# Optimization experiments

Hardware: AMD Instinct MI355X
Metric: run time of the kernel (lower is better)

The kernel has to match this reference:

```python
import jax, jax.numpy as jnp
import numpy as np

B, S, H = 2, 2048, 2048
NH, NKV, HD = 8, 2, 256
WIN = 512
EPS = 1e-6
WAV = 10000.0


def _rms_norm(x, scale=None, eps=EPS):
    # Gemma3n RMSNorm: normalize in float32 over last dim, optional learned scale.
    x32 = x.astype(jnp.float32)
    n = x32 * jax.lax.rsqrt(jnp.mean(x32 * x32, axis=-1, keepdims=True) + eps)
    if scale is not None:
        n = n * scale
    return n.astype(x.dtype)


def _rope(x):
    # keras-hub RotaryEmbedding (half-split rotation). x: [B, S, nheads, hd]
    s, hd = x.shape[1], x.shape[-1]
    inv_freq = 1.0 / (WAV ** (jnp.arange(0, hd, 2, dtype=jnp.float32) / hd))  # [hd/2]
    freqs = jnp.arange(s, dtype=jnp.float32)[:, None] * inv_freq[None, :]      # [S, hd/2]
    cos = jnp.cos(freqs)[None, :, None, :]
    sin = jnp.sin(freqs)[None, :, None, :]
    x1, x2 = jnp.split(x, 2, axis=-1)
    return jnp.concatenate([x1 * cos - x2 * sin, x2 * cos + x1 * sin], axis=-1)


def setup_inputs() -> dict:
    key = jax.random.key(0)
    ks = jax.random.split(key, 8)
    hidden_states = jax.random.normal(ks[0], (B, S, H), dtype=jnp.float32)
    # causal mask [B, S, S]
    causal = jnp.tril(jnp.ones((S, S), dtype=bool))
    attention_mask = jnp.broadcast_to(causal[None], (B, S, S))
    sd = 1.0 / np.sqrt(H)
    Wq = jax.random.normal(ks[1], (H, NH * HD), dtype=jnp.float32) * sd
    Wk = jax.random.normal(ks[2], (H, NKV * HD), dtype=jnp.float32) * sd
    Wv = jax.random.normal(ks[3], (H, NKV * HD), dtype=jnp.float32) * sd
    Wo = jax.random.normal(ks[4], (NH * HD, H), dtype=jnp.float32) * (1.0 / np.sqrt(NH * HD))
    q_scale = jnp.ones((HD,), jnp.float32) + 0.02 * jax.random.normal(ks[5], (HD,), dtype=jnp.float32)
    k_scale = jnp.ones((HD,), jnp.float32) + 0.02 * jax.random.normal(ks[6], (HD,), dtype=jnp.float32)
    return {"hidden_states": hidden_states, "attention_mask": attention_mask,
            "Wq": Wq, "Wk": Wk, "Wv": Wv, "Wo": Wo,
            "q_scale": q_scale, "k_scale": k_scale}


def reference(hidden_states, attention_mask, Wq, Wk, Wv, Wo, q_scale, k_scale):
    b, s, _ = hidden_states.shape
    # Q: proj -> per-head RMSNorm -> RoPE -> [B, NH, S, HD]
    q = (hidden_states @ Wq).reshape(b, s, NH, HD)
    q = jnp.transpose(_rope(_rms_norm(q, q_scale)), (0, 2, 1, 3))
    # K: proj -> RMSNorm -> RoPE; V: proj -> RMSNorm (no scale, no RoPE)
    k = (hidden_states @ Wk).reshape(b, s, NKV, HD)
    k = jnp.transpose(_rope(_rms_norm(k, k_scale)), (0, 2, 1, 3))
    v = jnp.transpose(_rms_norm((hidden_states @ Wv).reshape(b, s, NKV, HD)), (0, 2, 1, 3))
    # GQA repeat_kv (groups = NH // NKV)
    g = NH // NKV
    k = jnp.repeat(k, g, axis=1)
    v = jnp.repeat(v, g, axis=1)
    # scores with scaling = 1.0 (as in source)
    scores = jnp.einsum('bhqd,bhkd->bhqk', q, k)
    # sliding-window band AND user causal mask
    idx = jnp.arange(s)
    band = jnp.abs(idx[:, None] - idx[None, :]) <= (WIN - 1)  # [S, S]
    mask = attention_mask.astype(bool) & band[None]           # [B, S, S]
    scores = jnp.where(mask[:, None], scores, -1e9)
    attn = jax.nn.softmax(scores, axis=-1)
    out = jnp.einsum('bhqk,bhkd->bhqd', attn, v)
    out = jnp.transpose(out, (0, 2, 1, 3)).reshape(b, s, NH * HD)
    return out @ Wo
```

## Files before the change

kernel.cpp:

```cpp
#include <hip/hip_runtime.h>
#include <cstdint>
#include <cstddef>

typedef unsigned short u16;
typedef float floatx4 __attribute__((ext_vector_type(4)));
typedef __bf16 bf16x8 __attribute__((ext_vector_type(8)));

__device__ __forceinline__ u16 f2bf(float f) {
  union { float f; unsigned u; } v;
  v.f = f;
  unsigned u = v.u;
  u += 0x7FFFu + ((u >> 16) & 1u);
  return (u16)(u >> 16);
}
__device__ __forceinline__ float bf2f(u16 h) {
  union { unsigned u; float f; } v;
  v.u = ((unsigned)h) << 16;
  return v.f;
}

#define GLL16(g, l)                                                       \
  __builtin_amdgcn_global_load_lds(                                       \
      (const __attribute__((address_space(1))) void*)(g),                 \
      (__attribute__((address_space(3))) void*)(l), 16, 0, 0)


__global__ __launch_bounds__(256) void splitbf(const float* __restrict__ in,
                                               u16* __restrict__ oh,
                                               u16* __restrict__ ol, int n8) {
  int idx = blockIdx.x * 256 + threadIdx.x;
  if (idx >= n8) return;
  float x[8];
  *(float4*)&x[0] = *(const float4*)(in + (size_t)idx * 8);
  *(float4*)&x[4] = *(const float4*)(in + (size_t)idx * 8 + 4);
  u16 h[8], l[8];
#pragma unroll
  for (int j = 0; j < 8; ++j) {
    h[j] = f2bf(x[j]);
    l[j] = f2bf(x[j] - bf2f(h[j]));
  }
  *(uint4*)(oh + (size_t)idx * 8) = *(const uint4*)h;
  *(uint4*)(ol + (size_t)idx * 8) = *(const uint4*)l;
}

__global__ __launch_bounds__(256) void wtrans(const float* __restrict__ in,
                                              u16* __restrict__ out, int R,
                                              int C) {
  __shared__ u16 T[64][80];
  const int t = threadIdx.x;
  const int r0 = blockIdx.y * 64;
  const int c0 = blockIdx.x * 64;
#pragma unroll
  for (int p = 0; p < 4; ++p) {
    const int rl = (t >> 4) + p * 16;
    const int c4 = (t & 15) * 4;
    float4 v = *(const float4*)(in + (size_t)(r0 + rl) * C + c0 + c4);
    T[c4 + 0][rl] = f2bf(v.x);
    T[c4 + 1][rl] = f2bf(v.y);
    T[c4 + 2][rl] = f2bf(v.z);
    T[c4 + 3][rl] = f2bf(v.w);
  }
  __syncthreads();
#pragma unroll
  for (int p = 0; p < 2; ++p) {
    const int cl = (t >> 3) + p * 32;
    const int r8 = (t & 7) * 8;
    *(uint4*)(out + (size_t)(c0 + cl) * R + r0 + r8) =
        *(const uint4*)&T[cl][r8];
  }
}

__global__ __launch_bounds__(256) void gemm_bf16s2(
    const u16* __restrict__ Ah, const u16* __restrict__ Al,
    const u16* __restrict__ Bt, float* __restrict__ C, int M, int N, int K) {
  __shared__ u16 Ash[2][4096], Asl[2][4096], Bs[2][4096];
  const int tid = threadIdx.x;
  const int lane = tid & 63;
  const int wid = tid >> 6;
  const int g = lane >> 4, lc = lane & 15;
  const int gsw = g ^ ((lc >> 1) & 3);
  const int lbs = lc * 32 + gsw * 8;
  const int nwg = gridDim.x * gridDim.y;
  const int lin = blockIdx.y * gridDim.x + blockIdx.x;
  const int swz = (lin & 7) * (nwg >> 3) + (lin >> 3);
  const int bm = (swz / gridDim.x) * 128, bn = (swz % gridDim.x) * 128;
  const int wr = (wid >> 1) * 64, wc = (wid & 1) * 64;
  const int xk8 = (((tid & 3) ^ ((tid >> 3) & 3)) * 8);
  const size_t aoff = (size_t)(bm + (tid >> 2)) * K + xk8;
  const size_t boff = (size_t)(bn + (tid >> 2)) * K + xk8;

  floatx4 acc[4][4];
#pragma unroll
  for (int i = 0; i < 4; ++i)
#pragma unroll
    for (int j = 0; j < 4; ++j) acc[i][j] = floatx4{0.f, 0.f, 0.f, 0.f};

  GLL16(Ah + aoff, Ash[0] + tid * 8);
  GLL16(Ah + aoff + (size_t)64 * K, Ash[0] + 2048 + tid * 8);
  GLL16(Al + aoff, Asl[0] + tid * 8);
  GLL16(Al + aoff + (size_t)64 * K, Asl[0] + 2048 + tid * 8);
  GLL16(Bt + boff, Bs[0] + tid * 8);
  GLL16(Bt + boff + (size_t)64 * K, Bs[0] + 2048 + tid * 8);
  int cur = 0;

  for (int k0 = 0; k0 < K; k0 += 32) {
    __syncthreads();
    if (k0 + 32 < K) {
      const int kn = k0 + 32;
      GLL16(Ah + aoff + kn, Ash[cur ^ 1] + tid * 8);
      GLL16(Ah + aoff + (size_t)64 * K + kn, Ash[cur ^ 1] + 2048 + tid * 8);
      GLL16(Al + aoff + kn, Asl[cur ^ 1] + tid * 8);
      GLL16(Al + aoff + (size_t)64 * K + kn, Asl[cur ^ 1] + 2048 + tid * 8);
      GLL16(Bt + boff + kn, Bs[cur ^ 1] + tid * 8);
      GLL16(Bt + boff + (size_t)64 * K + kn, Bs[cur ^ 1] + 2048 + tid * 8);
    }
    bf16x8 afh[4], afl[4], bfr[4];
#pragma unroll
    for (int m = 0; m < 4; ++m) {
      afh[m] = *(const bf16x8*)(Ash[cur] + (wr + m * 16) * 32 + lbs);
      afl[m] = *(const bf16x8*)(Asl[cur] + (wr + m * 16) * 32 + lbs);
    }
#pragma unroll
    for (int n = 0; n < 4; ++n)
      bfr[n] = *(const bf16x8*)(Bs[cur] + (wc + n * 16) * 32 + lbs);
#pragma unroll
    for (int m = 0; m < 4; ++m)
#pragma unroll
      for (int n = 0; n < 4; ++n) {
        acc[m][n] = __builtin_amdgcn_mfma_f32_16x16x32_bf16(afh[m], bfr[n],
                                                            acc[m][n], 0, 0, 0);
        acc[m][n] = __builtin_amdgcn_mfma_f32_16x16x32_bf16(afl[m], bfr[n],
                                                            acc[m][n], 0, 0, 0);
      }
    cur ^= 1;
  }
#pragma unroll
  for (int m = 0; m < 4; ++m)
#pragma unroll
    for (int n = 0; n < 4; ++n) {
      float* Cp = C + (size_t)(bm + wr + m * 16 + g * 4) * N + bn + wc +
                  n * 16 + lc;
#pragma unroll
      for (int r = 0; r < 4; ++r) Cp[(size_t)r * N] = acc[m][n][r];
    }
}

__global__ __launch_bounds__(256) void gemm_bf16(const u16* __restrict__ A,
                                                 const u16* __restrict__ Bt,
                                                 float* __restrict__ C, int M,
                                                 int N, int K) {
  __shared__ u16 As[2][4096];
  __shared__ u16 Bs[2][4096];
  const int tid = threadIdx.x;
  const int lane = tid & 63;
  const int wid = tid >> 6;
  const int g = lane >> 4, lc = lane & 15;
  const int gsw = g ^ ((lc >> 1) & 3);
  const int lbs = lc * 32 + gsw * 8;
  const int nwg = gridDim.x * gridDim.y;
  const int lin = blockIdx.y * gridDim.x + blockIdx.x;
  const int swz = (lin & 7) * (nwg >> 3) + (lin >> 3);
  const int bm = (swz / gridDim.x) * 128, bn = (swz % gridDim.x) * 128;
  const int wr = (wid >> 1) * 64, wc = (wid & 1) * 64;
  const int xk8 = (((tid & 3) ^ ((tid >> 3) & 3)) * 8);
  const u16* Ag = A + (size_t)(bm + (tid >> 2)) * K + xk8;
  const u16* Bg = Bt + (size_t)(bn + (tid >> 2)) * K + xk8;

  floatx4 acc[4][4];
#pragma unroll
  for (int i = 0; i < 4; ++i)
#pragma unroll
    for (int j = 0; j < 4; ++j) acc[i][j] = floatx4{0.f, 0.f, 0.f, 0.f};

  GLL16(Ag, As[0] + tid * 8);
  GLL16(Ag + (size_t)64 * K, As[0] + 2048 + tid * 8);
  GLL16(Bg, Bs[0] + tid * 8);
  GLL16(Bg + (size_t)64 * K, Bs[0] + 2048 + tid * 8);
  int cur = 0;

  for (int k0 = 0; k0 < K; k0 += 32) {
    __syncthreads();
    if (k0 + 32 < K) {
      const int kn = k0 + 32;
      GLL16(Ag + kn, As[cur ^ 1] + tid * 8);
      GLL16(Ag + (size_t)64 * K + kn, As[cur ^ 1] + 2048 + tid * 8);
      GLL16(Bg + kn, Bs[cur ^ 1] + tid * 8);
      GLL16(Bg + (size_t)64 * K + kn, Bs[cur ^ 1] + 2048 + tid * 8);
    }
    bf16x8 af[4], bfr[4];
#pragma unroll
    for (int m = 0; m < 4; ++m)
      af[m] = *(const bf16x8*)(As[cur] + (wr + m * 16) * 32 + lbs);
#pragma unroll
    for (int n = 0; n < 4; ++n)
      bfr[n] = *(const bf16x8*)(Bs[cur] + (wc + n * 16) * 32 + lbs);
#pragma unroll
    for (int m = 0; m < 4; ++m)
#pragma unroll
      for (int n = 0; n < 4; ++n)
        acc[m][n] = __builtin_amdgcn_mfma_f32_16x16x32_bf16(af[m], bfr[n],
                                                            acc[m][n], 0, 0, 0);
    cur ^= 1;
  }
#pragma unroll
  for (int m = 0; m < 4; ++m)
#pragma unroll
    for (int n = 0; n < 4; ++n) {
      float* Cp = C + (size_t)(bm + wr + m * 16 + g * 4) * N + bn + wc +
                  n * 16 + lc;
#pragma unroll
      for (int r = 0; r < 4; ++r) Cp[(size_t)r * N] = acc[m][n][r];
    }
}

__global__ __launch_bounds__(128) void trigtab(float* __restrict__ ct,
                                               float* __restrict__ st) {
  const int s = blockIdx.x, fi = threadIdx.x;
  const float invf = expf((float)fi * (-9.210340371976184f / 128.f));
  float sv, cv;
  sincosf((float)s * invf, &sv, &cv);
  ct[s * 128 + fi] = cv;
  st[s * 128 + fi] = sv;
}

__global__ __launch_bounds__(256) void rmsrope2(
    const float* __restrict__ qproj, const float* __restrict__ kvproj,
    u16* __restrict__ qph, u16* __restrict__ qpl, u16* __restrict__ kph,
    u16* __restrict__ kpl, u16* __restrict__ vpk,
    const float* __restrict__ q_scale, const float* __restrict__ k_scale,
    const float* __restrict__ ct, const float* __restrict__ st) {
  __shared__ u16 nh[32][264], nl[32][264];
  const int t = threadIdx.x, lane = t & 63, w = t >> 6;
  const int blk = blockIdx.x;
  const int slot = blk % 12;
  const int rt = blk / 12;
  const int bs0 = rt * 32;
  const int b = bs0 >> 11;
  const int s0 = bs0 & 2047;
  const float* srcb;
  const float* scale = nullptr;
  int srccol, srcstride;
  bool rope;
  if (slot < 8) {
    srcb = qproj;
    srccol = slot * 256;
    srcstride = 2048;
    scale = q_scale;
    rope = true;
  } else if (slot < 10) {
    srcb = kvproj;
    srccol = (slot - 8) * 256;
    srcstride = 1024;
    scale = k_scale;
    rope = true;
  } else {
    srcb = kvproj;
    srccol = 512 + (slot - 10) * 256;
    srcstride = 1024;
    rope = false;
  }
  const int d0 = lane * 4;
  float4 sc4 = make_float4(1.f, 1.f, 1.f, 1.f);
  if (scale) sc4 = *(const float4*)(scale + d0);
  const int fi4 = (lane & 31) * 4;

#pragma unroll
  for (int rr = 0; rr < 8; ++rr) {
    const int r = w * 8 + rr;
    const int s = s0 + r;
    float4 x = *(const float4*)(srcb + (size_t)(bs0 + r) * srcstride + srccol +
                                d0);
    float ss = x.x * x.x + x.y * x.y + x.z * x.z + x.w * x.w;
#pragma unroll
    for (int off = 32; off; off >>= 1) ss += __shfl_xor(ss, off);
    const float inv = rsqrtf(ss * (1.f / 256.f) + 1e-6f);
    float4 n;
    n.x = x.x * inv * sc4.x;
    n.y = x.y * inv * sc4.y;
    n.z = x.z * inv * sc4.z;
    n.w = x.w * inv * sc4.w;
    if (rope) {
      float4 p;
      p.x = __shfl_xor(n.x, 32);
      p.y = __shfl_xor(n.y, 32);
      p.z = __shfl_xor(n.z, 32);
      p.w = __shfl_xor(n.w, 32);
      const float4 cv = *(const float4*)(ct + s * 128 + fi4);
      const float4 sv = *(const float4*)(st + s * 128 + fi4);
      if (lane < 32) {
        n.x = n.x * cv.x - p.x * sv.x;
        n.y = n.y * cv.y - p.y * sv.y;
        n.z = n.z * cv.z - p.z * sv.z;
        n.w = n.w * cv.w - p.w * sv.w;
      } else {
        n.x = n.x * cv.x + p.x * sv.x;
        n.y = n.y * cv.y + p.y * sv.y;
        n.z = n.z * cv.z + p.z * sv.z;
        n.w = n.w * cv.w + p.w * sv.w;
      }
    }
    const float nv[4] = {n.x, n.y, n.z, n.w};
#pragma unroll
    for (int j = 0; j < 4; ++j) {
      const u16 hh = f2bf(nv[j]);
      nh[r][d0 + j] = hh;
      nl[r][d0 + j] = f2bf(nv[j] - bf2f(hh));
    }
  }
  __syncthreads();

  if (slot < 8) {
    u16* dh = qph + (((size_t)(b * 8 + slot) * 128 + (s0 >> 4)) * 4096);
    u16* dl = qpl + (((size_t)(b * 8 + slot) * 128 + (s0 >> 4)) * 4096);
#pragma unroll
    for (int p = 0; p < 4; ++p) {
      const int gi = p * 256 + t;
      const int tile = gi >> 9, kc = (gi >> 6) & 7, lc2 = (gi >> 2) & 15,
                gg = gi & 3;
      const int row = tile * 16 + lc2, col = kc * 32 + gg * 8;
      *(uint4*)(dh + (size_t)gi * 8) = *(const uint4*)&nh[row][col];
      *(uint4*)(dl + (size_t)gi * 8) = *(const uint4*)&nl[row][col];
    }
  } else if (slot < 10) {
    const int kvh = slot - 8;
    u16* dh = kph + (((size_t)(b * 2 + kvh) * 64 + (s0 >> 5)) * 8192);
    u16* dl = kpl + (((size_t)(b * 2 + kvh) * 64 + (s0 >> 5)) * 8192);
#pragma unroll
    for (int p = 0; p < 4; ++p) {
      const int gi = p * 256 + t;
      const int kc = gi >> 7, hi = (gi >> 6) & 1, lc2 = (gi >> 2) & 15,
                gg = gi & 3;
      const int ggs = gg ^ ((lc2 >> 1) & 3);
      const int row = hi * 16 + lc2, col = kc * 32 + gg * 8;
      const size_t off = kc * 1024 + hi * 512 + lc2 * 32 + ggs * 8;
      *(uint4*)(dh + off) = *(const uint4*)&nh[row][col];
      *(uint4*)(dl + off) = *(const uint4*)&nl[row][col];
    }
  } else {
    const int kvh = slot - 10;
    u16* dv = vpk + (((size_t)(b * 2 + kvh) * 64 + (s0 >> 5)) * 8192);
#pragma unroll
    for (int p = 0; p < 4; ++p) {
      const int gi = p * 256 + t;
      const int di = gi >> 6, lc2 = (gi >> 2) & 15, gg = gi & 3;
      const int ggs = gg ^ ((lc2 >> 1) & 3);
      u16 tmp[8];
#pragma unroll
      for (int e = 0; e < 8; ++e) tmp[e] = nh[gg * 8 + e][di * 16 + lc2];
      *(uint4*)(dv + (size_t)(di * 512 + lc2 * 32 + ggs * 8)) =
          *(const uint4*)tmp;
    }
  }
}

__global__ __launch_bounds__(512) void attn_mfma4(
    const u16* __restrict__ qph, const u16* __restrict__ qpl,
    const u16* __restrict__ kph, const u16* __restrict__ kpl,
    const u16* __restrict__ vpk, u16* __restrict__ attnb) {
  __shared__ u16 KhB[2][8192], KlB[2][8192], VB[2][8192];
  __shared__ u16 Pl[8][640];
  const int tid = threadIdx.x, lane = tid & 63, wid = tid >> 6;
  const int g = lane >> 4, lc = lane & 15;
  const int lbu = lc * 32 + g * 8;
  const int lbs = lc * 32 + (g ^ ((lc >> 1) & 3)) * 8;
  const int lin = blockIdx.x;
  const int swz = (lin & 7) * 32 + (lin >> 3);
  const int qt = swz & 15;
  const int h = (swz >> 4) & 7;
  const int b = swz >> 7;
  const int kvh = h >> 2;
  const int i0b = qt * 128;
  const int i0 = i0b + wid * 16;

  bf16x8 qfh[8], qfl[8];
  {
    const size_t qtb = ((size_t)(b * 8 + h) * 128 + (i0 >> 4)) * 4096 + lbu;
#pragma unroll
    for (int kc = 0; kc < 8; ++kc) {
      qfh[kc] = *(const bf16x8*)(qph + qtb + kc * 512);
      qfl[kc] = *(const bf16x8*)(qpl + qtb + kc * 512);
    }
  }
  floatx4 o[16];
#pragma unroll
  for (int d = 0; d < 16; ++d) o[d] = floatx4{0.f, 0.f, 0.f, 0.f};
  float m_[4] = {-1e20f, -1e20f, -1e20f, -1e20f};
  float l_[4] = {0.f, 0.f, 0.f, 0.f};
  u16* pw = Pl[wid];

  const int jlo = (i0b >= 512) ? i0b - 512 : 0;
  const int nt = (i0b + 128 - jlo) >> 5;
  const size_t kvbase = (size_t)(b * 2 + kvh) * 64;
  const int t0 = jlo >> 5;

  {
    const size_t tb = (kvbase + t0) * 8192;
    GLL16(kph + tb + tid * 8, KhB[0] + tid * 8);
    GLL16(kph + tb + 4096 + tid * 8, KhB[0] + 4096 + tid * 8);
    GLL16(kpl + tb + tid * 8, KlB[0] + tid * 8);
    GLL16(kpl + tb + 4096 + tid * 8, KlB[0] + 4096 + tid * 8);
    GLL16(vpk + tb + tid * 8, VB[0] + tid * 8);
    GLL16(vpk + tb + 4096 + tid * 8, VB[0] + 4096 + tid * 8);
  }
  int cur = 0;

  for (int t = 0; t < nt; ++t) {
    __syncthreads();
    if (t + 1 < nt) {
      const size_t tb = (kvbase + t0 + t + 1) * 8192;
      GLL16(kph + tb + tid * 8, KhB[cur ^ 1] + tid * 8);
      GLL16(kph + tb + 4096 + tid * 8, KhB[cur ^ 1] + 4096 + tid * 8);
      GLL16(kpl + tb + tid * 8, KlB[cur ^ 1] + tid * 8);
      GLL16(kpl + tb + 4096 + tid * 8, KlB[cur ^ 1] + 4096 + tid * 8);
      GLL16(vpk + tb + tid * 8, VB[cur ^ 1] + tid * 8);
      GLL16(vpk + tb + 4096 + tid * 8, VB[cur ^ 1] + 4096 + tid * 8);
    }
    const int j0 = jlo + t * 32;
    if (!(j0 > i0 + 15 || j0 + 31 < i0 - 511)) {
      const u16* Kh = KhB[cur];
      const u16* Kl = KlB[cur];
      floatx4 s0 = floatx4{0.f, 0.f, 0.f, 0.f};
      floatx4 s1 = floatx4{0.f, 0.f, 0.f, 0.f};
      __builtin_amdgcn_s_setprio(1);
#pragma unroll
      for (int kc = 0; kc < 8; ++kc) {
        const bf16x8 kh0 = *(const bf16x8*)(Kh + kc * 1024 + lbs);
        const bf16x8 kh1 = *(const bf16x8*)(Kh + kc * 1024 + 512 + lbs);
        const bf16x8 kl0 = *(const bf16x8*)(Kl + kc * 1024 + lbs);
        const bf16x8 kl1 = *(const bf16x8*)(Kl + kc * 1024 + 512 + lbs);
        s0 = __builtin_amdgcn_mfma_f32_16x16x32_bf16(qfh[kc], kh0, s0, 0, 0, 0);
        s0 = __builtin_amdgcn_mfma_f32_16x16x32_bf16(qfh[kc], kl0, s0, 0, 0, 0);
        s0 = __builtin_amdgcn_mfma_f32_16x16x32_bf16(qfl[kc], kh0, s0, 0, 0, 0);
        s1 = __builtin_amdgcn_mfma_f32_16x16x32_bf16(qfh[kc], kh1, s1, 0, 0, 0);
        s1 = __builtin_amdgcn_mfma_f32_16x16x32_bf16(qfh[kc], kl1, s1, 0, 0, 0);
        s1 = __builtin_amdgcn_mfma_f32_16x16x32_bf16(qfl[kc], kh1, s1, 0, 0, 0);
      }
      __builtin_amdgcn_s_setprio(0);
      if (!(j0 + 31 <= i0 && (i0 + 15) - j0 <= 511)) {
        const int ja = j0 + lc, jb_ = j0 + 16 + lc;
#pragma unroll
        for (int r = 0; r < 4; ++r) {
          const int i = i0 + g * 4 + r;
          if (ja > i || i - ja > 511) s0[r] = -1e30f;
          if (jb_ > i || i - jb_ > 511) s1[r] = -1e30f;
        }
      }
      float rmax[4], p0[4], p1[4], sc[4], rs[4];
#pragma unroll
      for (int r = 0; r < 4; ++r) rmax[r] = fmaxf(s0[r], s1[r]);
#pragma unroll
      for (int off = 1; off < 16; off <<= 1)
#pragma unroll
        for (int r = 0; r < 4; ++r)
          rmax[r] = fmaxf(rmax[r], __shfl_xor(rmax[r], off));
#pragma unroll
      for (int r = 0; r < 4; ++r) {
        const float mn = fmaxf(m_[r], rmax[r]);
        sc[r] = __expf(m_[r] - mn);
        m_[r] = mn;
        p0[r] = __expf(s0[r] - mn);
        p1[r] = __expf(s1[r] - mn);
        rs[r] = p0[r] + p1[r];
      }
#pragma unroll
      for (int off = 1; off < 16; off <<= 1)
#pragma unroll
        for (int r = 0; r < 4; ++r) rs[r] += __shfl_xor(rs[r], off);
#pragma unroll
      for (int r = 0; r < 4; ++r) l_[r] = l_[r] * sc[r] + rs[r];
#pragma unroll
      for (int r = 0; r < 4; ++r) {
        pw[(g * 4 + r) * 40 + lc] = f2bf(p0[r]);
        pw[(g * 4 + r) * 40 + 16 + lc] = f2bf(p1[r]);
      }
#pragma unroll
      for (int d = 0; d < 16; ++d)
#pragma unroll
        for (int r = 0; r < 4; ++r) o[d][r] *= sc[r];
      const bf16x8 pf = *(const bf16x8*)(pw + lc * 40 + g * 8);
      const u16* Vt = VB[cur];
      __builtin_amdgcn_s_setprio(1);
#pragma unroll
      for (int d = 0; d < 16; ++d)
        o[d] = __builtin_amdgcn_mfma_f32_16x16x32_bf16(
            pf, *(const bf16x8*)(Vt + d * 512 + lbs), o[d], 0, 0, 0);
      __builtin_amdgcn_s_setprio(0);
    }
    cur ^= 1;
  }
  float rinv[4];
#pragma unroll
  for (int r = 0; r < 4; ++r) rinv[r] = 1.f / l_[r];
  u16* ob = attnb + (size_t)(b * 2048 + i0 + g * 4) * 2048 + h * 256 + lc;
#pragma unroll
  for (int d = 0; d < 16; ++d)
#pragma unroll
    for (int r = 0; r < 4; ++r)
      ob[(size_t)r * 2048 + d * 16] = f2bf(o[d][r] * rinv[r]);
}

extern "C" void kernel_launch(void* const* d_in, const int* in_sizes, int n_in,
                              void* d_out, int out_size, void* d_ws,
                              size_t ws_size, hipStream_t stream) {
  (void)in_sizes;
  (void)n_in;
  (void)out_size;
  (void)ws_size;
  const float* X = (const float*)d_in[0];
  const float* Wq = (const float*)d_in[2];
  const float* Wk = (const float*)d_in[3];
  const float* Wv = (const float*)d_in[4];
  const float* Wo = (const float*)d_in[5];
  const float* qs = (const float*)d_in[6];
  const float* ks = (const float*)d_in[7];
  float* out = (float*)d_out;
  char* ws = (char*)d_ws;

  float* kvproj = (float*)(ws);
  u16* attnb = (u16*)(ws);
  u16* Xh = (u16*)(ws + 16777216);
  u16* qph = Xh;
  u16* Xl = (u16*)(ws + 33554432);
  u16* qpl = Xl;
  u16* Wth = (u16*)(ws + 50331648);
  u16* kph = (u16*)(ws + 50331648);
  u16* kpl = (u16*)(ws + 54525952);
  u16* vpk = (u16*)(ws + 58720256);
  float* ct = (float*)(ws + 62914560);
  float* st = (float*)(ws + 63963136);
  u16* Wot = (u16*)(ws + 75497472);
  float* qproj = out;

  splitbf<<<4096, 256, 0, stream>>>(X, Xh, Xl, 1048576);
  wtrans<<<dim3(32, 32), 256, 0, stream>>>(Wq, Wth, 2048, 2048);
  wtrans<<<dim3(8, 32), 256, 0, stream>>>(Wk, Wth + (size_t)2048 * 2048, 2048,
                                          512);
  wtrans<<<dim3(8, 32), 256, 0, stream>>>(Wv, Wth + (size_t)2560 * 2048, 2048,
                                          512);
  wtrans<<<dim3(32, 32), 256, 0, stream>>>(Wo, Wot, 2048, 2048);
  gemm_bf16s2<<<dim3(16, 32), 256, 0, stream>>>(Xh, Xl, Wth, qproj, 4096, 2048,
                                                2048);
  gemm_bf16s2<<<dim3(8, 32), 256, 0, stream>>>(
      Xh, Xl, Wth + (size_t)2048 * 2048, kvproj, 4096, 1024, 2048);
  trigtab<<<2048, 128, 0, stream>>>(ct, st);
  rmsrope2<<<12 * 128, 256, 0, stream>>>(qproj, kvproj, qph, qpl, kph, kpl,
                                         vpk, qs, ks, ct, st);
  attn_mfma4<<<256, 512, 0, stream>>>(qph, qpl, kph, kpl, vpk, attnb);
  gemm_bf16<<<dim3(16, 32), 256, 0, stream>>>(attnb, Wot, out, 4096, 2048,
                                              2048);
}
```

Before: 299.1 us.

## Merge prep kernels, fuse QKV GEMMs, split score accumulators, stage attention output

```diff
diff --git a/kernel.cpp b/kernel.cpp
--- a/kernel.cpp
+++ b/kernel.cpp
@@ -24,32 +24,54 @@
       (const __attribute__((address_space(1))) void*)(g),                 \
       (__attribute__((address_space(3))) void*)(l), 16, 0, 0)
 
-
-__global__ __launch_bounds__(256) void splitbf(const float* __restrict__ in,
-                                               u16* __restrict__ oh,
-                                               u16* __restrict__ ol, int n8) {
-  int idx = blockIdx.x * 256 + threadIdx.x;
-  if (idx >= n8) return;
-  float x[8];
-  *(float4*)&x[0] = *(const float4*)(in + (size_t)idx * 8);
-  *(float4*)&x[4] = *(const float4*)(in + (size_t)idx * 8 + 4);
-  u16 h[8], l[8];
-#pragma unroll
-  for (int j = 0; j < 8; ++j) {
-    h[j] = f2bf(x[j]);
-    l[j] = f2bf(x[j] - bf2f(h[j]));
-  }
-  *(uint4*)(oh + (size_t)idx * 8) = *(const uint4*)h;
-  *(uint4*)(ol + (size_t)idx * 8) = *(const uint4*)l;
-}
-
-__global__ __launch_bounds__(256) void wtrans(const float* __restrict__ in,
-                                              u16* __restrict__ out, int R,
-                                              int C) {
+__global__ __launch_bounds__(256) void prep_all(
+    const float* __restrict__ X, u16* __restrict__ Xh, u16* __restrict__ Xl,
+    const float* __restrict__ Wq, const float* __restrict__ Wk,
+    const float* __restrict__ Wv, const float* __restrict__ Wo,
+    u16* __restrict__ Wth, u16* __restrict__ Wot, float* __restrict__ ct,
+    float* __restrict__ st) {
   __shared__ u16 T[64][80];
-  const int t = threadIdx.x;
-  const int r0 = blockIdx.y * 64;
-  const int c0 = blockIdx.x * 64;
+  const int blk = blockIdx.x, t = threadIdx.x;
+  if (blk < 4096) {
+    const int idx = blk * 256 + t;
+    float x[8];
+    *(float4*)&x[0] = *(const float4*)(X + (size_t)idx * 8);
+    *(float4*)&x[4] = *(const float4*)(X + (size_t)idx * 8 + 4);
+    u16 h[8], l[8];
+#pragma unroll
+    for (int j = 0; j < 8; ++j) {
+      h[j] = f2bf(x[j]);
+      l[j] = f2bf(x[j] - bf2f(h[j]));
+    }
+    *(uint4*)(Xh + (size_t)idx * 8) = *(const uint4*)h;
+    *(uint4*)(Xl + (size_t)idx * 8) = *(const uint4*)l;
+    return;
+  }
+  if (blk >= 6656) {
+    const int idx = (blk - 6656) * 256 + t;
+    const int s = idx >> 7, fi = idx & 127;
+    const float invf = expf((float)fi * (-9.210340371976184f / 128.f));
+    float sv, cv;
+    sincosf((float)s * invf, &sv, &cv);
+    ct[idx] = cv;
+    st[idx] = sv;
+    return;
+  }
+  const float* in;
+  u16* out;
+  int C, tt, gx, gy;
+  if (blk < 5120) {
+    in = Wq; out = Wth; C = 2048; tt = blk - 4096; gx = tt & 31; gy = tt >> 5;
+  } else if (blk < 5376) {
+    in = Wk; out = Wth + (size_t)2048 * 2048; C = 512; tt = blk - 5120;
+    gx = tt & 7; gy = tt >> 3;
+  } else if (blk < 5632) {
+    in = Wv; out = Wth + (size_t)2560 * 2048; C = 512; tt = blk - 5376;
+    gx = tt & 7; gy = tt >> 3;
+  } else {
+    in = Wo; out = Wot; C = 2048; tt = blk - 5632; gx = tt & 31; gy = tt >> 5;
+  }
+  const int r0 = gy * 64, c0 = gx * 64;
 #pragma unroll
   for (int p = 0; p < 4; ++p) {
     const int rl = (t >> 4) + p * 16;
@@ -65,14 +87,15 @@
   for (int p = 0; p < 2; ++p) {
     const int cl = (t >> 3) + p * 32;
     const int r8 = (t & 7) * 8;
-    *(uint4*)(out + (size_t)(c0 + cl) * R + r0 + r8) =
+    *(uint4*)(out + (size_t)(c0 + cl) * 2048 + r0 + r8) =
         *(const uint4*)&T[cl][r8];
   }
 }
 
-__global__ __launch_bounds__(256) void gemm_bf16s2(
+__global__ __launch_bounds__(256) void gemm_qkv2(
     const u16* __restrict__ Ah, const u16* __restrict__ Al,
-    const u16* __restrict__ Bt, float* __restrict__ C, int M, int N, int K) {
+    const u16* __restrict__ Bt_all, float* __restrict__ Cq,
+    float* __restrict__ Ckv, int K) {
   __shared__ u16 Ash[2][4096], Asl[2][4096], Bs[2][4096];
   const int tid = threadIdx.x;
   const int lane = tid & 63;
@@ -80,10 +103,18 @@
   const int g = lane >> 4, lc = lane & 15;
   const int gsw = g ^ ((lc >> 1) & 3);
   const int lbs = lc * 32 + gsw * 8;
-  const int nwg = gridDim.x * gridDim.y;
-  const int lin = blockIdx.y * gridDim.x + blockIdx.x;
-  const int swz = (lin & 7) * (nwg >> 3) + (lin >> 3);
-  const int bm = (swz / gridDim.x) * 128, bn = (swz % gridDim.x) * 128;
+  const int lin = blockIdx.x;
+  const u16* Bt;
+  float* C;
+  int N, nwg, gridx, lin_s;
+  if (lin < 512) {
+    Bt = Bt_all; C = Cq; N = 2048; nwg = 512; gridx = 16; lin_s = lin;
+  } else {
+    Bt = Bt_all + (size_t)2048 * 2048; C = Ckv; N = 1024; nwg = 256;
+    gridx = 8; lin_s = lin - 512;
+  }
+  const int swz = (lin_s & 7) * (nwg >> 3) + (lin_s >> 3);
+  const int bm = (swz / gridx) * 128, bn = (swz % gridx) * 128;
   const int wr = (wid >> 1) * 64, wc = (wid & 1) * 64;
   const int xk8 = (((tid & 3) ^ ((tid >> 3) & 3)) * 8);
   const size_t aoff = (size_t)(bm + (tid >> 2)) * K + xk8;
@@ -213,16 +244,6 @@
     }
 }
 
-__global__ __launch_bounds__(128) void trigtab(float* __restrict__ ct,
-                                               float* __restrict__ st) {
-  const int s = blockIdx.x, fi = threadIdx.x;
-  const float invf = expf((float)fi * (-9.210340371976184f / 128.f));
-  float sv, cv;
-  sincosf((float)s * invf, &sv, &cv);
-  ct[s * 128 + fi] = cv;
-  st[s * 128 + fi] = sv;
-}
-
 __global__ __launch_bounds__(256) void rmsrope2(
     const float* __restrict__ qproj, const float* __restrict__ kvproj,
     u16* __restrict__ qph, u16* __restrict__ qpl, u16* __restrict__ kph,
@@ -242,21 +263,13 @@
   int srccol, srcstride;
   bool rope;
   if (slot < 8) {
-    srcb = qproj;
-    srccol = slot * 256;
-    srcstride = 2048;
-    scale = q_scale;
+    srcb = qproj; srccol = slot * 256; srcstride = 2048; scale = q_scale;
     rope = true;
   } else if (slot < 10) {
-    srcb = kvproj;
-    srccol = (slot - 8) * 256;
-    srcstride = 1024;
-    scale = k_scale;
-    rope = true;
+    srcb = kvproj; srccol = (slot - 8) * 256; srcstride = 1024;
+    scale = k_scale; rope = true;
   } else {
-    srcb = kvproj;
-    srccol = 512 + (slot - 10) * 256;
-    srcstride = 1024;
+    srcb = kvproj; srccol = 512 + (slot - 10) * 256; srcstride = 1024;
     rope = false;
   }
   const int d0 = lane * 4;
@@ -353,12 +366,14 @@
   }
 }
 
-__global__ __launch_bounds__(512) void attn_mfma4(
+__global__ __launch_bounds__(512) void attn_mfma5(
     const u16* __restrict__ qph, const u16* __restrict__ qpl,
     const u16* __restrict__ kph, const u16* __restrict__ kpl,
     const u16* __restrict__ vpk, u16* __restrict__ attnb) {
-  __shared__ u16 KhB[2][8192], KlB[2][8192], VB[2][8192];
-  __shared__ u16 Pl[8][640];
+  __shared__ u16 SH[54272];
+  u16* const KhB = SH;
+  u16* const KlB = SH + 16384;
+  u16* const VB = SH + 32768;
   const int tid = threadIdx.x, lane = tid & 63, wid = tid >> 6;
   const int g = lane >> 4, lc = lane & 15;
   const int lbu = lc * 32 + g * 8;
@@ -386,7 +401,7 @@
   for (int d = 0; d < 16; ++d) o[d] = floatx4{0.f, 0.f, 0.f, 0.f};
   float m_[4] = {-1e20f, -1e20f, -1e20f, -1e20f};
   float l_[4] = {0.f, 0.f, 0.f, 0.f};
-  u16* pw = Pl[wid];
+  u16* pw = SH + 49152 + wid * 640;
 
   const int jlo = (i0b >= 512) ? i0b - 512 : 0;
   const int nt = (i0b + 128 - jlo) >> 5;
@@ -395,12 +410,12 @@
 
   {
     const size_t tb = (kvbase + t0) * 8192;
-    GLL16(kph + tb + tid * 8, KhB[0] + tid * 8);
-    GLL16(kph + tb + 4096 + tid * 8, KhB[0] + 4096 + tid * 8);
-    GLL16(kpl + tb + tid * 8, KlB[0] + tid * 8);
-    GLL16(kpl + tb + 4096 + tid * 8, KlB[0] + 4096 + tid * 8);
-    GLL16(vpk + tb + tid * 8, VB[0] + tid * 8);
-    GLL16(vpk + tb + 4096 + tid * 8, VB[0] + 4096 + tid * 8);
+    GLL16(kph + tb + tid * 8, KhB + tid * 8);
+    GLL16(kph + tb + 4096 + tid * 8, KhB + 4096 + tid * 8);
+    GLL16(kpl + tb + tid * 8, KlB + tid * 8);
+    GLL16(kpl + tb + 4096 + tid * 8, KlB + 4096 + tid * 8);
+    GLL16(vpk + tb + tid * 8, VB + tid * 8);
+    GLL16(vpk + tb + 4096 + tid * 8, VB + 4096 + tid * 8);
   }
   int cur = 0;
 
@@ -408,19 +423,20 @@
     __syncthreads();
     if (t + 1 < nt) {
       const size_t tb = (kvbase + t0 + t + 1) * 8192;
-      GLL16(kph + tb + tid * 8, KhB[cur ^ 1] + tid * 8);
-      GLL16(kph + tb + 4096 + tid * 8, KhB[cur ^ 1] + 4096 + tid * 8);
-      GLL16(kpl + tb + tid * 8, KlB[cur ^ 1] + tid * 8);
-      GLL16(kpl + tb + 4096 + tid * 8, KlB[cur ^ 1] + 4096 + tid * 8);
-      GLL16(vpk + tb + tid * 8, VB[cur ^ 1] + tid * 8);
-      GLL16(vpk + tb + 4096 + tid * 8, VB[cur ^ 1] + 4096 + tid * 8);
+      const int nb = (cur ^ 1) * 8192;
+      GLL16(kph + tb + tid * 8, KhB + nb + tid * 8);
+      GLL16(kph + tb + 4096 + tid * 8, KhB + nb + 4096 + tid * 8);
+      GLL16(kpl + tb + tid * 8, KlB + nb + tid * 8);
+      GLL16(kpl + tb + 4096 + tid * 8, KlB + nb + 4096 + tid * 8);
+      GLL16(vpk + tb + tid * 8, VB + nb + tid * 8);
+      GLL16(vpk + tb + 4096 + tid * 8, VB + nb + 4096 + tid * 8);
     }
     const int j0 = jlo + t * 32;
     if (!(j0 > i0 + 15 || j0 + 31 < i0 - 511)) {
-      const u16* Kh = KhB[cur];
-      const u16* Kl = KlB[cur];
-      floatx4 s0 = floatx4{0.f, 0.f, 0.f, 0.f};
-      floatx4 s1 = floatx4{0.f, 0.f, 0.f, 0.f};
+      const u16* Kh = KhB + cur * 8192;
+      const u16* Kl = KlB + cur * 8192;
+      floatx4 s0h = floatx4{0.f, 0.f, 0.f, 0.f}, s0x = s0h, s0y = s0h;
+      floatx4 s1h = s0h, s1x = s0h, s1y = s0h;
       __builtin_amdgcn_s_setprio(1);
 #pragma unroll
       for (int kc = 0; kc < 8; ++kc) {
@@ -428,14 +444,16 @@
         const bf16x8 kh1 = *(const bf16x8*)(Kh + kc * 1024 + 512 + lbs);
         const bf16x8 kl0 = *(const bf16x8*)(Kl + kc * 1024 + lbs);
         const bf16x8 kl1 = *(const bf16x8*)(Kl + kc * 1024 + 512 + lbs);
-        s0 = __builtin_amdgcn_mfma_f32_16x16x32_bf16(qfh[kc], kh0, s0, 0, 0, 0);
-        s0 = __builtin_amdgcn_mfma_f32_16x16x32_bf16(qfh[kc], kl0, s0, 0, 0, 0);
-        s0 = __builtin_amdgcn_mfma_f32_16x16x32_bf16(qfl[kc], kh0, s0, 0, 0, 0);
-        s1 = __builtin_amdgcn_mfma_f32_16x16x32_bf16(qfh[kc], kh1, s1, 0, 0, 0);
-        s1 = __builtin_amdgcn_mfma_f32_16x16x32_bf16(qfh[kc], kl1, s1, 0, 0, 0);
-        s1 = __builtin_amdgcn_mfma_f32_16x16x32_bf16(qfl[kc], kh1, s1, 0, 0, 0);
+        s0h = __builtin_amdgcn_mfma_f32_16x16x32_bf16(qfh[kc], kh0, s0h, 0, 0, 0);
+        s1h = __builtin_amdgcn_mfma_f32_16x16x32_bf16(qfh[kc], kh1, s1h, 0, 0, 0);
+        s0x = __builtin_amdgcn_mfma_f32_16x16x32_bf16(qfh[kc], kl0, s0x, 0, 0, 0);
+        s1x = __builtin_amdgcn_mfma_f32_16x16x32_bf16(qfh[kc], kl1, s1x, 0, 0, 0);
+        s0y = __builtin_amdgcn_mfma_f32_16x16x32_bf16(qfl[kc], kh0, s0y, 0, 0, 0);
+        s1y = __builtin_amdgcn_mfma_f32_16x16x32_bf16(qfl[kc], kh1, s1y, 0, 0, 0);
       }
       __builtin_amdgcn_s_setprio(0);
+      floatx4 s0 = s0h + s0x + s0y;
+      floatx4 s1 = s1h + s1x + s1y;
       if (!(j0 + 31 <= i0 && (i0 + 15) - j0 <= 511)) {
         const int ja = j0 + lc, jb_ = j0 + 16 + lc;
 #pragma unroll
@@ -478,7 +496,7 @@
 #pragma unroll
         for (int r = 0; r < 4; ++r) o[d][r] *= sc[r];
       const bf16x8 pf = *(const bf16x8*)(pw + lc * 40 + g * 8);
-      const u16* Vt = VB[cur];
+      const u16* Vt = VB + cur * 8192;
       __builtin_amdgcn_s_setprio(1);
 #pragma unroll
       for (int d = 0; d < 16; ++d)
@@ -491,12 +509,21 @@
   float rinv[4];
 #pragma unroll
   for (int r = 0; r < 4; ++r) rinv[r] = 1.f / l_[r];
-  u16* ob = attnb + (size_t)(b * 2048 + i0 + g * 4) * 2048 + h * 256 + lc;
+  __syncthreads();
+  u16* ow = SH + wid * 4224;
 #pragma unroll
   for (int d = 0; d < 16; ++d)
 #pragma unroll
     for (int r = 0; r < 4; ++r)
-      ob[(size_t)r * 2048 + d * 16] = f2bf(o[d][r] * rinv[r]);
+      ow[(g * 4 + r) * 264 + d * 16 + lc] = f2bf(o[d][r] * rinv[r]);
+  u16* orow = attnb + ((size_t)(b * 2048 + i0) * 2048 + h * 256);
+#pragma unroll
+  for (int p = 0; p < 8; ++p) {
+    const int gi = p * 64 + lane;
+    const int row = gi >> 5, ch = gi & 31;
+    *(uint4*)(orow + (size_t)row * 2048 + ch * 8) =
+        *(const uint4*)(ow + row * 264 + ch * 8);
+  }
 }
 
 extern "C" void kernel_launch(void* const* d_in, const int* in_sizes, int n_in,
@@ -531,21 +558,12 @@
   u16* Wot = (u16*)(ws + 75497472);
   float* qproj = out;
 
-  splitbf<<<4096, 256, 0, stream>>>(X, Xh, Xl, 1048576);
-  wtrans<<<dim3(32, 32), 256, 0, stream>>>(Wq, Wth, 2048, 2048);
-  wtrans<<<dim3(8, 32), 256, 0, stream>>>(Wk, Wth + (size_t)2048 * 2048, 2048,
-                                          512);
-  wtrans<<<dim3(8, 32), 256, 0, stream>>>(Wv, Wth + (size_t)2560 * 2048, 2048,
-                                          512);
-  wtrans<<<dim3(32, 32), 256, 0, stream>>>(Wo, Wot, 2048, 2048);
-  gemm_bf16s2<<<dim3(16, 32), 256, 0, stream>>>(Xh, Xl, Wth, qproj, 4096, 2048,
-                                                2048);
-  gemm_bf16s2<<<dim3(8, 32), 256, 0, stream>>>(
-      Xh, Xl, Wth + (size_t)2048 * 2048, kvproj, 4096, 1024, 2048);
-  trigtab<<<2048, 128, 0, stream>>>(ct, st);
+  prep_all<<<7680, 256, 0, stream>>>(X, Xh, Xl, Wq, Wk, Wv, Wo, Wth, Wot, ct,
+                                     st);
+  gemm_qkv2<<<768, 256, 0, stream>>>(Xh, Xl, Wth, qproj, kvproj, 2048);
   rmsrope2<<<12 * 128, 256, 0, stream>>>(qproj, kvproj, qph, qpl, kph, kpl,
                                          vpk, qs, ks, ct, st);
-  attn_mfma4<<<256, 512, 0, stream>>>(qph, qpl, kph, kpl, vpk, attnb);
+  attn_mfma5<<<256, 512, 0, stream>>>(qph, qpl, kph, kpl, vpk, attnb);
   gemm_bf16<<<dim3(16, 32), 256, 0, stream>>>(attnb, Wot, out, 4096, 2048,
                                               2048);
 }
```

After: 259.7 us. 13.2% less time.
